# Kernel tuning notes

Hardware: AMD Instinct MI355X
Metric: run time of the kernel (lower is better)

## Reference

```python
import jax, jax.numpy as jnp
import numpy as np

GROUPS = 8
EPS = 1e-5


def group_norm(x, gamma, beta):
    # x: (b, c, h, w); normalize per sample over each group of c//GROUPS channels and all spatial dims
    b, c, h, w = x.shape
    xg = x.reshape(b, GROUPS, c // GROUPS, h, w)
    mean = jnp.mean(xg, axis=(2, 3, 4), keepdims=True)
    var = jnp.var(xg, axis=(2, 3, 4), keepdims=True)
    xn = ((xg - mean) * jax.lax.rsqrt(var + EPS)).reshape(b, c, h, w)
    return xn * gamma[None, :, None, None] + beta[None, :, None, None]


def setup_inputs() -> dict:
    key = jax.random.key(0)
    k1, k2, k3 = jax.random.split(key, 3)
    b, c, h, w = 32, 256, 32, 32
    x = jax.random.normal(k1, (b, c, h, w), dtype=jnp.float32)
    qkv_w = jax.random.normal(k2, (3 * c, c), dtype=jnp.float32) * 0.02
    qkv_b = jnp.zeros((3 * c,), dtype=jnp.float32)
    out_w = jax.random.normal(k3, (c, c), dtype=jnp.float32) * 0.02
    out_b = jnp.zeros((c,), dtype=jnp.float32)
    gn_gamma = jnp.ones((c,), dtype=jnp.float32)
    gn_beta = jnp.zeros((c,), dtype=jnp.float32)
    return {"x": x, "gn_gamma": gn_gamma, "gn_beta": gn_beta,
            "qkv_w": qkv_w, "qkv_b": qkv_b, "out_w": out_w, "out_b": out_b}


def reference(x, gn_gamma, gn_beta, qkv_w, qkv_b, out_w, out_b):
    b, c, h, w = x.shape
    xn = group_norm(x, gn_gamma, gn_beta)
    # 1x1 conv == per-pixel linear: (b,c,h,w) x (3c,c) -> (b,3c,h,w)
    qkv = jnp.einsum('bchw,dc->bdhw', xn, qkv_w) + qkv_b[None, :, None, None]
    q, k, v = jnp.split(qkv, 3, axis=1)
    # (b, c, h, w) -> (b, hw, c)
    def tok(t):
        return t.transpose(0, 2, 3, 1).reshape(b, h * w, c)
    q, k, v = tok(q), tok(k), tok(v)
    scale = 1.0 / jnp.sqrt(jnp.asarray(c, dtype=x.dtype))
    scores = jnp.einsum('bnc,bmc->bnm', q, k) * scale  # (b, hw, hw)
    attn = jax.nn.softmax(scores, axis=-1)
    out = jnp.einsum('bnm,bmc->bnc', attn, v)  # (b, hw, c)
    out = out.reshape(b, h, w, c).transpose(0, 3, 1, 2)  # (b, c, h, w)
    out = jnp.einsum('bchw,dc->bdhw', out, out_w) + out_b[None, :, None, None]
    return out + x
```

## Files before the change

kernel.cpp:

```cpp
#include <hip/hip_runtime.h>
#include <hip/hip_bf16.h>
#include <stdint.h>


typedef __bf16 bf16_t;
typedef __bf16 bf16x4 __attribute__((ext_vector_type(4)));
typedef __bf16 bf16x8 __attribute__((ext_vector_type(8)));
typedef float f32x16 __attribute__((ext_vector_type(16)));
typedef _Float16 f16x4 __attribute__((ext_vector_type(4)));

#define MFMA32(a, b, c) __builtin_amdgcn_mfma_f32_32x32x16_bf16((a), (b), (c), 0, 0, 0)
#define GLL16(g, l)                                                                      \
    __builtin_amdgcn_global_load_lds((const __attribute__((address_space(1))) void*)(g), \
                                     (__attribute__((address_space(3))) void*)(l), 16, 0, 0)
#define WAITV4 asm volatile("s_waitcnt vmcnt(4)" ::: "memory")
#define WAITV0 asm volatile("s_waitcnt vmcnt(0)" ::: "memory")
#define SBAR   __builtin_amdgcn_s_barrier()

#define QSCALE 0.0901684400555f

__device__ inline uint32_t pack2(float a, float b) {
    union { uint32_t u; __bf16 h[2]; } w;
    w.h[0] = (__bf16)a; w.h[1] = (__bf16)b;
    return w.u;
}

__global__ void cast_w(const float* __restrict__ s1, bf16_t* __restrict__ d1, int n1,
                       const float* __restrict__ s2, bf16_t* __restrict__ d2, int n2) {
    int i = blockIdx.x * blockDim.x + threadIdx.x;
    int stride = gridDim.x * blockDim.x;
    for (int k = i; k < n1; k += stride) d1[k] = (bf16_t)s1[k];
    for (int k = i; k < n2; k += stride) d2[k] = (bf16_t)s2[k];
}

__global__ __launch_bounds__(256) void gn_kernel(const float* __restrict__ x,
                                                 const float* __restrict__ gamma,
                                                 const float* __restrict__ beta,
                                                 bf16_t* __restrict__ xn) {
    extern __shared__ char gsm[];
    float* red = (float*)(gsm + 65536);
    int bg = blockIdx.x, b = bg >> 3, g = bg & 7;
    const float* base = x + (size_t)(b * 256 + g * 32) * 1024;
    int tid = threadIdx.x;

    float s = 0.f, ss = 0.f;
    #pragma unroll 4
    for (int c = 0; c < 32; c++) {
        float4 v = *(const float4*)(base + c * 1024 + tid * 4);
        s += v.x + v.y + v.z + v.w;
        ss += v.x * v.x + v.y * v.y + v.z * v.z + v.w * v.w;
        f16x4 h = {(_Float16)v.x, (_Float16)v.y, (_Float16)v.z, (_Float16)v.w};
        *(f16x4*)(gsm + c * 2048 + ((tid * 8) ^ ((c & 7) << 4))) = h;
    }
    for (int off = 32; off; off >>= 1) { s += __shfl_down(s, off); ss += __shfl_down(ss, off); }
    if ((tid & 63) == 0) { red[tid >> 6] = s; red[4 + (tid >> 6)] = ss; }
    __syncthreads();
    float S = red[0] + red[1] + red[2] + red[3];
    float SS = red[4] + red[5] + red[6] + red[7];
    float mean = S * (1.0f / 32768.0f);
    float var = SS * (1.0f / 32768.0f) - mean * mean;
    float rstd = rsqrtf(var + 1e-5f);

    int c = tid & 31;
    float gam = gamma[g * 32 + c] * rstd;
    float bet = beta[g * 32 + c] - mean * gam;
    bf16_t* dst = xn + (size_t)(b * 1024) * 256 + g * 32 + c;
    #pragma unroll 4
    for (int it = 0; it < 128; it++) {
        int p = it * 8 + (tid >> 5);
        _Float16 hv = *(_Float16*)(gsm + c * 2048 + ((p * 2) ^ ((c & 7) << 4)));
        dst[(size_t)p * 256] = (bf16_t)((float)hv * gam + bet);
    }
}

__global__ __launch_bounds__(256, 1) void gemm_qkv(const bf16_t* __restrict__ xn,
                                                   const bf16_t* __restrict__ wq,
                                                   const float* __restrict__ qkv_b,
                                                   bf16_t* __restrict__ qb,
                                                   bf16_t* __restrict__ kb,
                                                   bf16_t* __restrict__ vt) {
    extern __shared__ char smem[];
    char* As = smem;
    int tid = threadIdx.x, wv = tid >> 6, lane = tid & 63;
    int l31 = lane & 31, hi = lane >> 5;
    int t0 = blockIdx.x * 128;
    const char* asrc = (const char*)xn + (size_t)t0 * 512;
    const char* wsrc = (const char*)wq;

    {
        int u = lane & 31, rofs = lane >> 5;
        #pragma unroll
        for (int t = 0; t < 16; t++) {
            int r0 = t * 8 + wv * 2;
            int r = r0 + rofs;
            GLL16(asrc + (size_t)r * 512 + ((u ^ (r & 31)) * 16), As + r0 * 512);
        }
    }
    auto stage_B = [&](int nt) {
        char* Bd = smem + 65536 + (nt & 1) * 32768;
        int u = lane & 31, rofs = lane >> 5;
        #pragma unroll
        for (int t = 0; t < 8; t++) {
            int r0 = wv * 16 + t * 2;
            int r = r0 + rofs;
            GLL16(wsrc + (size_t)(nt * 64 + r) * 512 + ((u ^ (r & 31)) * 16), Bd + r0 * 512);
        }
    };
    stage_B(0);
    WAITV0; SBAR;

    int wm = wv >> 1, wd = wv & 1;
    int bb = t0 >> 10, pos0 = t0 & 1023;

    for (int nt = 0; nt < 12; nt++) {
        if (nt < 11) stage_B(nt + 1);
        const char* Bs = smem + 65536 + (nt & 1) * 32768;
        f32x16 acc0 = {}, acc1 = {};
        if (nt < 8) {
            __builtin_amdgcn_s_setprio(1);
            #pragma unroll
            for (int ks = 0; ks < 16; ks++) {
                int col = ks * 32 + hi * 16;
                bf16x8 a0 = *(const bf16x8*)(As + (wm * 64 + l31) * 512 + (col ^ (l31 << 4)));
                bf16x8 a1 = *(const bf16x8*)(As + (wm * 64 + 32 + l31) * 512 + (col ^ (l31 << 4)));
                bf16x8 b  = *(const bf16x8*)(Bs + (wd * 32 + l31) * 512 + (col ^ (l31 << 4)));
                acc0 = MFMA32(a0, b, acc0);
                acc1 = MFMA32(a1, b, acc1);
            }
            __builtin_amdgcn_s_setprio(0);
            int d = nt * 64 + wd * 32 + l31;
            bool isq = nt < 4;
            float bias = qkv_b[d];
            bf16_t* dst = isq ? qb : kb;
            int dd = isq ? d : d - 256;
            float sc = isq ? QSCALE : 1.0f;
            #pragma unroll
            for (int ms = 0; ms < 2; ms++) {
                #pragma unroll
                for (int r = 0; r < 16; r++) {
                    float v = ms ? acc1[r] : acc0[r];
                    int tok = t0 + wm * 64 + ms * 32 + (r & 3) + 8 * (r >> 2) + 4 * hi;
                    dst[(size_t)tok * 256 + dd] = (bf16_t)((v + bias) * sc);
                }
            }
        } else {
            __builtin_amdgcn_s_setprio(1);
            #pragma unroll
            for (int ks = 0; ks < 16; ks++) {
                int col = ks * 32 + hi * 16;
                bf16x8 a0 = *(const bf16x8*)(As + (wm * 64 + l31) * 512 + (col ^ (l31 << 4)));
                bf16x8 a1 = *(const bf16x8*)(As + (wm * 64 + 32 + l31) * 512 + (col ^ (l31 << 4)));
                bf16x8 b  = *(const bf16x8*)(Bs + (wd * 32 + l31) * 512 + (col ^ (l31 << 4)));
                acc0 = MFMA32(b, a0, acc0);
                acc1 = MFMA32(b, a1, acc1);
            }
            __builtin_amdgcn_s_setprio(0);
            int dbase = (nt - 8) * 64 + wd * 32;
            #pragma unroll
            for (int ms = 0; ms < 2; ms++) {
                int pos = pos0 + wm * 64 + ms * 32 + l31;
                #pragma unroll
                for (int r = 0; r < 16; r++) {
                    float v = ms ? acc1[r] : acc0[r];
                    int d = dbase + (r & 3) + 8 * (r >> 2) + 4 * hi;
                    vt[(size_t)bb * 262144 + (size_t)d * 1024 + pos] =
                        (bf16_t)(v + qkv_b[512 + d]);
                }
            }
        }
        if (nt < 11) { WAITV0; SBAR; }
    }
}

__global__ __launch_bounds__(512, 1) void attn_kernel(const bf16_t* __restrict__ qb,
                                                      const bf16_t* __restrict__ kb,
                                                      const bf16_t* __restrict__ vt,
                                                      bf16_t* __restrict__ ao) {
    extern __shared__ char smem[];
    int tid = threadIdx.x, i = blockIdx.x;
    int b = (i & 7) + ((i >> 6) << 3);
    int qt = (i >> 3) & 7;
    int wv = tid >> 6, lane = tid & 63, l31 = lane & 31, hi = lane >> 5;
    int qgrp = wv & 3, dh = wv >> 2;

    const char* kbase = (const char*)kb + (size_t)b * 524288;
    const char* vbase = (const char*)vt + (size_t)b * 524288;

    int qg = qt * 128 + qgrp * 32 + l31;
    const char* qsrc = (const char*)qb + (size_t)(b * 1024 + qg) * 512;
    bf16x8 qf[16];
    #pragma unroll
    for (int ks = 0; ks < 16; ks++) qf[ks] = *(const bf16x8*)(qsrc + ks * 32 + hi * 16);

    f32x16 o[4] = {};
    float mrun = -1e30f, lrun = 0.f;

    auto stage = [&](int ch) {
        char* Kd = smem + (ch % 3) * 32768;
        char* Vd = Kd + 16384;
        int j0 = ch * 32;
        #pragma unroll
        for (int p = 0; p < 2; p++) {
            int Ls = (tid << 4) + (p << 13);
            int s = Ls ^ (((Ls >> 9) & 31) << 4);
            int dstoff = wv * 1024 + p * 8192;
            GLL16(kbase + (size_t)(j0 + (Ls >> 9)) * 512 + (s & 511), Kd + dstoff);
            GLL16(vbase + (size_t)(s >> 6) * 2048 + j0 * 2 + (s & 63), Vd + dstoff);
        }
    };

    stage(0);
    stage(1);

    for (int ch = 0; ch < 32; ch++) {
        if (ch < 31) { WAITV4; } else { WAITV0; }
        SBAR;
        if (ch + 2 < 32) stage(ch + 2);
        const char* Ks = smem + (ch % 3) * 32768;
        const char* Vs = Ks + 16384;

        f32x16 se = {}, so2 = {};
        __builtin_amdgcn_s_setprio(1);
        #pragma unroll
        for (int ks = 0; ks < 16; ks += 2) {
            int c0 = ks * 32 + hi * 16;
            int c1 = c0 + 32;
            bf16x8 k0 = *(const bf16x8*)(Ks + l31 * 512 + (c0 ^ (l31 << 4)));
            bf16x8 k1 = *(const bf16x8*)(Ks + l31 * 512 + (c1 ^ (l31 << 4)));
            se = MFMA32(k0, qf[ks], se);
            so2 = MFMA32(k1, qf[ks + 1], so2);
        }
        __builtin_amdgcn_s_setprio(0);
        f32x16 sv = se + so2;

        float mc = -1e30f;
        #pragma unroll
        for (int r = 0; r < 16; r++) mc = fmaxf(mc, sv[r]);
        mc = fmaxf(mc, __shfl_xor(mc, 32));
        float mo = mrun;
        float mn = (mc <= mo + 8.0f) ? mo : mc;
        float rs = 0.f;
        #pragma unroll
        for (int r = 0; r < 16; r++) {
            sv[r] = exp2f(sv[r] - mn);
            rs += sv[r];
        }
        rs += __shfl_xor(rs, 32);
        float al = exp2f(mo - mn);
        lrun = lrun * al + rs;
        mrun = mn;
        if (__any(mn != mo)) {
            #pragma unroll
            for (int dt = 0; dt < 4; dt++) o[dt] = o[dt] * al;
        }

        #pragma unroll
        for (int pk = 0; pk < 2; pk++) {
            uint32_t A0 = pack2(sv[pk * 8 + 0], sv[pk * 8 + 1]);
            uint32_t A1 = pack2(sv[pk * 8 + 2], sv[pk * 8 + 3]);
            uint32_t B0 = pack2(sv[pk * 8 + 4], sv[pk * 8 + 5]);
            uint32_t B1 = pack2(sv[pk * 8 + 6], sv[pk * 8 + 7]);
            asm volatile("v_permlane32_swap_b32 %0, %1" : "+v"(B0), "+v"(A0));
            asm volatile("v_permlane32_swap_b32 %0, %1" : "+v"(B1), "+v"(A1));
            union { bf16x8 v; uint32_t u[4]; } pw;
            pw.u[0] = A0; pw.u[1] = A1; pw.u[2] = B0; pw.u[3] = B1;
            __builtin_amdgcn_s_setprio(1);
            #pragma unroll
            for (int dt = 0; dt < 4; dt++) {
                int d = dh * 128 + dt * 32 + l31;
                int a = (d * 64 + pk * 32 + hi * 16) ^ (((d >> 3) & 31) << 4);
                bf16x8 vf = *(const bf16x8*)(Vs + a);
                o[dt] = MFMA32(vf, pw.v, o[dt]);
            }
            __builtin_amdgcn_s_setprio(0);
        }
    }

    float inv = 1.0f / lrun;
    char* aod = (char*)ao + (size_t)(b * 1024 + qg) * 512 + dh * 256;
    #pragma unroll
    for (int dt = 0; dt < 4; dt++) {
        #pragma unroll
        for (int rg = 0; rg < 4; rg++) {
            bf16x4 w;
            #pragma unroll
            for (int r = 0; r < 4; r++) w[r] = (bf16_t)(o[dt][rg * 4 + r] * inv);
            *(bf16x4*)(aod + dt * 64 + rg * 16 + hi * 8) = w;
        }
    }
}

__global__ __launch_bounds__(256, 1) void gemm_out(const bf16_t* __restrict__ wo,
                                                   const bf16_t* __restrict__ ao,
                                                   const float* __restrict__ out_b,
                                                   const float* __restrict__ x,
                                                   float* __restrict__ out) {
    extern __shared__ char smem[];
    char* Bs = smem;
    int tid = threadIdx.x, wv = tid >> 6, lane = tid & 63;
    int l31 = lane & 31, hi = lane >> 5;
    int t0 = blockIdx.x * 128;
    const char* bsrc = (const char*)ao + (size_t)t0 * 512;
    const char* wsrc = (const char*)wo;

    {
        int u = lane & 31, rofs = lane >> 5;
        #pragma unroll
        for (int t = 0; t < 16; t++) {
            int r0 = t * 8 + wv * 2;
            int r = r0 + rofs;
            GLL16(bsrc + (size_t)r * 512 + ((u ^ (r & 31)) * 16), Bs + r0 * 512);
        }
    }
    auto stage_W = [&](int ct) {
        char* Wd = smem + 65536 + (ct & 1) * 32768;
        int u = lane & 31, rofs = lane >> 5;
        #pragma unroll
        for (int t = 0; t < 8; t++) {
            int r0 = wv * 16 + t * 2;
            int r = r0 + rofs;
            GLL16(wsrc + (size_t)(ct * 64 + r) * 512 + ((u ^ (r & 31)) * 16), Wd + r0 * 512);
        }
    };
    stage_W(0);
    WAITV0; SBAR;

    int wm = wv >> 1, wc = wv & 1;
    int bb = t0 >> 10, pos0 = t0 & 1023;

    for (int ct = 0; ct < 4; ct++) {
        if (ct < 3) stage_W(ct + 1);
        const char* Ws = smem + 65536 + (ct & 1) * 32768;
        f32x16 acc0 = {}, acc1 = {};
        __builtin_amdgcn_s_setprio(1);
        #pragma unroll
        for (int ks = 0; ks < 16; ks++) {
            int col = ks * 32 + hi * 16;
            bf16x8 w  = *(const bf16x8*)(Ws + (wc * 32 + l31) * 512 + (col ^ (l31 << 4)));
            bf16x8 b0 = *(const bf16x8*)(Bs + (wm * 64 + l31) * 512 + (col ^ (l31 << 4)));
            bf16x8 b1 = *(const bf16x8*)(Bs + (wm * 64 + 32 + l31) * 512 + (col ^ (l31 << 4)));
            acc0 = MFMA32(w, b0, acc0);
            acc1 = MFMA32(w, b1, acc1);
        }
        __builtin_amdgcn_s_setprio(0);
        #pragma unroll
        for (int ms = 0; ms < 2; ms++) {
            int pos = pos0 + wm * 64 + ms * 32 + l31;
            #pragma unroll
            for (int r = 0; r < 16; r++) {
                float v = ms ? acc1[r] : acc0[r];
                int c = ct * 64 + wc * 32 + (r & 3) + 8 * (r >> 2) + 4 * hi;
                size_t idx = ((size_t)bb * 256 + c) * 1024 + pos;
                out[idx] = v + out_b[c] + x[idx];
            }
        }
        if (ct < 3) { WAITV0; SBAR; }
    }
}

extern "C" void kernel_launch(void* const* d_in, const int* in_sizes, int n_in,
                              void* d_out, int out_size, void* d_ws, size_t ws_size,
                              hipStream_t stream) {
    (void)in_sizes; (void)n_in; (void)out_size; (void)ws_size;
    const float* x      = (const float*)d_in[0];
    const float* gamma  = (const float*)d_in[1];
    const float* beta   = (const float*)d_in[2];
    const float* qkv_w  = (const float*)d_in[3];
    const float* qkv_b  = (const float*)d_in[4];
    const float* out_w  = (const float*)d_in[5];
    const float* out_b  = (const float*)d_in[6];
    float* out = (float*)d_out;

    char* ws = (char*)d_ws;
    const size_t MB16 = 16777216;
    bf16_t* xn  = (bf16_t*)(ws);
    bf16_t* qb  = (bf16_t*)(ws + 1 * MB16);
    bf16_t* kb  = (bf16_t*)(ws + 2 * MB16);
    bf16_t* vt  = (bf16_t*)(ws + 3 * MB16);
    bf16_t* ao  = (bf16_t*)(ws + 4 * MB16);
    bf16_t* wqb = (bf16_t*)(ws + 5 * MB16);
    bf16_t* wob = (bf16_t*)(ws + 5 * MB16 + 393216);

    cast_w<<<256, 256, 0, stream>>>(qkv_w, wqb, 196608, out_w, wob, 65536);
    gn_kernel<<<256, 256, 65600, stream>>>(x, gamma, beta, xn);
    gemm_qkv<<<256, 256, 131072, stream>>>(xn, wqb, qkv_b, qb, kb, vt);
    attn_kernel<<<256, 512, 98304, stream>>>(qb, kb, vt, ao);
    gemm_out<<<256, 256, 131072, stream>>>(wob, ao, out_b, x, out);
}
```

Measured before the change: 139.2 us.

## Split attention KV across wave halves with full head dim and merge partials

The attention kernel changes its wave split. Before, each pair of waves shared the same key chunk and split the output head dimension, so both recomputed QK^T. Now the two wave halves each take a different 32-key slice of a 64-key chunk, compute scores once, and accumulate all 256 output dims. This removes the duplicated QK^T MFMA work but doubles the accumulator registers, and it adds a shared-memory merge of the two online-softmax partials at the end. Staging moves from triple-buffered 32-key chunks to double-buffered 64-key chunks with an extra barrier per iteration, and the shared-memory request rises.

```diff
diff --git a/kernel.cpp b/kernel.cpp
--- a/kernel.cpp
+++ b/kernel.cpp
@@ -13,7 +13,7 @@
 #define GLL16(g, l)                                                                      \
     __builtin_amdgcn_global_load_lds((const __attribute__((address_space(1))) void*)(g), \
                                      (__attribute__((address_space(3))) void*)(l), 16, 0, 0)
-#define WAITV4 asm volatile("s_waitcnt vmcnt(4)" ::: "memory")
+#define WAITV8 asm volatile("s_waitcnt vmcnt(8)" ::: "memory")
 #define WAITV0 asm volatile("s_waitcnt vmcnt(0)" ::: "memory")
 #define SBAR   __builtin_amdgcn_s_barrier()
 
@@ -181,7 +181,7 @@
     int b = (i & 7) + ((i >> 6) << 3);
     int qt = (i >> 3) & 7;
     int wv = tid >> 6, lane = tid & 63, l31 = lane & 31, hi = lane >> 5;
-    int qgrp = wv & 3, dh = wv >> 2;
+    int qgrp = wv & 3, kh = wv >> 2;
 
     const char* kbase = (const char*)kb + (size_t)b * 524288;
     const char* vbase = (const char*)vt + (size_t)b * 524288;
@@ -192,41 +192,40 @@
     #pragma unroll
     for (int ks = 0; ks < 16; ks++) qf[ks] = *(const bf16x8*)(qsrc + ks * 32 + hi * 16);
 
-    f32x16 o[4] = {};
+    f32x16 o[8] = {};
     float mrun = -1e30f, lrun = 0.f;
 
     auto stage = [&](int ch) {
-        char* Kd = smem + (ch % 3) * 32768;
-        char* Vd = Kd + 16384;
-        int j0 = ch * 32;
-        #pragma unroll
-        for (int p = 0; p < 2; p++) {
+        char* Kd = smem + (ch & 1) * 65536;
+        char* Vd = Kd + 32768;
+        int j0 = ch * 64;
+        #pragma unroll
+        for (int p = 0; p < 4; p++) {
             int Ls = (tid << 4) + (p << 13);
             int s = Ls ^ (((Ls >> 9) & 31) << 4);
-            int dstoff = wv * 1024 + p * 8192;
+            int dstoff = wv * 1024 + (p << 13);
             GLL16(kbase + (size_t)(j0 + (Ls >> 9)) * 512 + (s & 511), Kd + dstoff);
-            GLL16(vbase + (size_t)(s >> 6) * 2048 + j0 * 2 + (s & 63), Vd + dstoff);
+            GLL16(vbase + (size_t)(s >> 7) * 2048 + j0 * 2 + (s & 127), Vd + dstoff);
         }
     };
 
     stage(0);
-    stage(1);
-
-    for (int ch = 0; ch < 32; ch++) {
-        if (ch < 31) { WAITV4; } else { WAITV0; }
+
+    for (int ch = 0; ch < 16; ch++) {
+        if (ch < 15) { stage(ch + 1); WAITV8; } else { WAITV0; }
         SBAR;
-        if (ch + 2 < 32) stage(ch + 2);
-        const char* Ks = smem + (ch % 3) * 32768;
-        const char* Vs = Ks + 16384;
-
+        const char* Ks = smem + (ch & 1) * 65536;
+        const char* Vs = Ks + 32768;
+
+        int krow = kh * 32 + l31;
         f32x16 se = {}, so2 = {};
         __builtin_amdgcn_s_setprio(1);
         #pragma unroll
         for (int ks = 0; ks < 16; ks += 2) {
             int c0 = ks * 32 + hi * 16;
             int c1 = c0 + 32;
-            bf16x8 k0 = *(const bf16x8*)(Ks + l31 * 512 + (c0 ^ (l31 << 4)));
-            bf16x8 k1 = *(const bf16x8*)(Ks + l31 * 512 + (c1 ^ (l31 << 4)));
+            bf16x8 k0 = *(const bf16x8*)(Ks + krow * 512 + (c0 ^ (l31 << 4)));
+            bf16x8 k1 = *(const bf16x8*)(Ks + krow * 512 + (c1 ^ (l31 << 4)));
             se = MFMA32(k0, qf[ks], se);
             so2 = MFMA32(k1, qf[ks + 1], so2);
         }
@@ -251,7 +250,7 @@
         mrun = mn;
         if (__any(mn != mo)) {
             #pragma unroll
-            for (int dt = 0; dt < 4; dt++) o[dt] = o[dt] * al;
+            for (int dt = 0; dt < 8; dt++) o[dt] = o[dt] * al;
         }
 
         #pragma unroll
@@ -266,26 +265,55 @@
             pw.u[0] = A0; pw.u[1] = A1; pw.u[2] = B0; pw.u[3] = B1;
             __builtin_amdgcn_s_setprio(1);
             #pragma unroll
-            for (int dt = 0; dt < 4; dt++) {
-                int d = dh * 128 + dt * 32 + l31;
-                int a = (d * 64 + pk * 32 + hi * 16) ^ (((d >> 3) & 31) << 4);
+            for (int dt = 0; dt < 8; dt++) {
+                int d = dt * 32 + l31;
+                int a = (d * 128 + kh * 64 + pk * 32 + hi * 16) ^ (((d >> 2) & 31) << 4);
                 bf16x8 vf = *(const bf16x8*)(Vs + a);
                 o[dt] = MFMA32(vf, pw.v, o[dt]);
             }
             __builtin_amdgcn_s_setprio(0);
         }
-    }
-
-    float inv = 1.0f / lrun;
-    char* aod = (char*)ao + (size_t)(b * 1024 + qg) * 512 + dh * 256;
-    #pragma unroll
-    for (int dt = 0; dt < 4; dt++) {
-        #pragma unroll
-        for (int rg = 0; rg < 4; rg++) {
-            bf16x4 w;
-            #pragma unroll
-            for (int r = 0; r < 4; r++) w[r] = (bf16_t)(o[dt][rg * 4 + r] * inv);
-            *(bf16x4*)(aod + dt * 64 + rg * 16 + hi * 8) = w;
+        SBAR;
+    }
+
+    __syncthreads();
+    float* mlb = (float*)(smem + 131072);
+    int sw = (l31 | (hi << 5)) & 31;
+    if (kh == 1) {
+        int base = qgrp * 32768 + lane * 512;
+        #pragma unroll
+        for (int dt = 0; dt < 8; dt++) {
+            #pragma unroll
+            for (int q = 0; q < 4; q++) {
+                float4 t = {o[dt][q * 4 + 0], o[dt][q * 4 + 1],
+                            o[dt][q * 4 + 2], o[dt][q * 4 + 3]};
+                *(float4*)(smem + ((base + dt * 64 + q * 16) ^ (sw << 4))) = t;
+            }
+        }
+        mlb[(qgrp * 64 + lane) * 2] = mrun;
+        mlb[(qgrp * 64 + lane) * 2 + 1] = lrun;
+    }
+    __syncthreads();
+    if (kh == 0) {
+        float m1 = mlb[(qgrp * 64 + lane) * 2];
+        float l1 = mlb[(qgrp * 64 + lane) * 2 + 1];
+        float mm = fmaxf(mrun, m1);
+        float a0 = exp2f(mrun - mm), a1 = exp2f(m1 - mm);
+        float linv = 1.0f / (lrun * a0 + l1 * a1);
+        int base = qgrp * 32768 + lane * 512;
+        char* aod = (char*)ao + (size_t)(b * 1024 + qg) * 512;
+        #pragma unroll
+        for (int dt = 0; dt < 8; dt++) {
+            #pragma unroll
+            for (int rg = 0; rg < 4; rg++) {
+                float4 o1 = *(const float4*)(smem + ((base + dt * 64 + rg * 16) ^ (sw << 4)));
+                bf16x4 w;
+                w[0] = (bf16_t)((o[dt][rg * 4 + 0] * a0 + o1.x * a1) * linv);
+                w[1] = (bf16_t)((o[dt][rg * 4 + 1] * a0 + o1.y * a1) * linv);
+                w[2] = (bf16_t)((o[dt][rg * 4 + 2] * a0 + o1.z * a1) * linv);
+                w[3] = (bf16_t)((o[dt][rg * 4 + 3] * a0 + o1.w * a1) * linv);
+                *(bf16x4*)(aod + dt * 64 + rg * 16 + hi * 8) = w;
+            }
         }
     }
 }
@@ -384,6 +412,6 @@
     cast_w<<<256, 256, 0, stream>>>(qkv_w, wqb, 196608, out_w, wob, 65536);
     gn_kernel<<<256, 256, 65600, stream>>>(x, gamma, beta, xn);
     gemm_qkv<<<256, 256, 131072, stream>>>(xn, wqb, qkv_b, qb, kb, vt);
-    attn_kernel<<<256, 512, 98304, stream>>>(qb, kb, vt, ao);
+    attn_kernel<<<256, 512, 133120, stream>>>(qb, kb, vt, ao);
     gemm_out<<<256, 256, 131072, stream>>>(wob, ao, out_b, x, out);
 }
```

After: 161.3 us. 1.16x slower.
